# Kernel tuning notes

Hardware: AMD Instinct MI355X
Metric: run time of the kernel (lower is better)

## Reference

```python
import jax, jax.numpy as jnp
import numpy as np

B, T, L, D, H = 8, 8192, 256, 512, 8
HD = D // H  # head_dim = 64


def setup_inputs() -> dict:
    key = jax.random.key(0)
    ks = jax.random.split(key, 6)
    s = 0.02
    return {
        "x": jax.random.normal(ks[0], (B, T, D), jnp.float32),
        "query": jax.random.normal(ks[1], (B, L, D), jnp.float32),
        "Wq": jax.random.normal(ks[2], (D, D), jnp.float32) * s,
        "bq": jnp.zeros((D,), jnp.float32),
        "Wkv": jax.random.normal(ks[3], (D, 2 * D), jnp.float32) * s,
        "bkv": jnp.zeros((2 * D,), jnp.float32),
        "Wproj": jax.random.normal(ks[4], (D, D), jnp.float32) * s,
        "bproj": jnp.zeros((D,), jnp.float32),
    }


def reference(x, query, Wq, bq, Wkv, bkv, Wproj, bproj):
    scale = HD ** (-0.5)
    # projections (weights stored [in, out]; equivalent to torch Linear with W.T)
    q = (query @ Wq + bq).reshape(B, L, H, HD).transpose(0, 2, 1, 3)   # [B,H,L,hd]
    kv = (x @ Wkv + bkv).reshape(B, T, 2, H, HD)
    k = kv[:, :, 0].transpose(0, 2, 1, 3)                              # [B,H,T,hd]
    v = kv[:, :, 1].transpose(0, 2, 1, 3)                              # [B,H,T,hd]
    # scaled dot-product attention, full L x T scores as in original
    attn = jnp.einsum("bhld,bhtd->bhlt", q * scale, k)                 # [B,H,L,T]
    attn = jax.nn.softmax(attn, axis=-1)
    out = jnp.einsum("bhlt,bhtd->bhld", attn, v)                       # [B,H,L,hd]
    out = out.transpose(0, 2, 1, 3).reshape(B, L, D)
    return out @ Wproj + bproj
```

## Files before the change

kernel.cpp:

```cpp
#include <hip/hip_runtime.h>
#include <hip/hip_bf16.h>
#include <cstdint>
#include <cstddef>

typedef __bf16 bf16_t;
typedef __bf16 bf16x8 __attribute__((ext_vector_type(8)));
typedef __bf16 bf16x4 __attribute__((ext_vector_type(4)));
typedef float  f32x4  __attribute__((ext_vector_type(4)));

#define DEVI __device__ __forceinline__

constexpr int B_ = 8, T_ = 8192, L_ = 256, D_ = 512, H_ = 8, HD_ = 64;
constexpr float SCALE_LOG2E = 0.125f * 1.44269504088896340736f;
constexpr int NSPLIT = 4;
constexpr int LOGNS = 2;

DEVI float fast_exp2(float x) {
#if __has_builtin(__builtin_amdgcn_exp2f)
  return __builtin_amdgcn_exp2f(x);
#else
  return exp2f(x);
#endif
}

DEVI void async16(void* lds_base, const void* gptr) {
#if __has_builtin(__builtin_amdgcn_global_load_lds)
  __builtin_amdgcn_global_load_lds(
      (__attribute__((address_space(1))) void*)gptr,
      (__attribute__((address_space(3))) void*)lds_base, 16, 0, 0);
#else
  ((bf16x8*)lds_base)[threadIdx.x & 63] = *(const bf16x8*)gptr;
#endif
}

__global__ __launch_bounds__(256) void prep(
    const float* __restrict__ x,     bf16_t* __restrict__ xb,
    const float* __restrict__ query, bf16_t* __restrict__ qin,
    const float* __restrict__ Wq,    bf16_t* __restrict__ wqT,
    const float* __restrict__ Wkv,   bf16_t* __restrict__ wkvT,
    const float* __restrict__ Wproj, bf16_t* __restrict__ wprojT) {
  __shared__ float tile[32][33];
  const int bid = blockIdx.x;
  const int tid = threadIdx.x;

  if (bid < 4096) {
    const int n4 = (B_ * T_ * D_) / 4;
    const int stride = 4096 * 256;
    for (int i = bid * 256 + tid; i < n4; i += stride) {
      float4 v = ((const float4*)x)[i];
      bf16x4 o;
      o[0] = (bf16_t)v.x; o[1] = (bf16_t)v.y; o[2] = (bf16_t)v.z; o[3] = (bf16_t)v.w;
      ((bf16x4*)xb)[i] = o;
    }
    return;
  }
  if (bid < 4352) {
    const int n4 = (B_ * L_ * D_) / 4;
    const int stride = 256 * 256;
    for (int i = (bid - 4096) * 256 + tid; i < n4; i += stride) {
      float4 v = ((const float4*)query)[i];
      bf16x4 o;
      o[0] = (bf16_t)v.x; o[1] = (bf16_t)v.y; o[2] = (bf16_t)v.z; o[3] = (bf16_t)v.w;
      ((bf16x4*)qin)[i] = o;
    }
    return;
  }

  const float* W; bf16_t* WT; int N; float scale; int idx;
  if (bid < 4608)      { idx = bid - 4352; W = Wq;    WT = wqT;    N = 512;  scale = SCALE_LOG2E; }
  else if (bid < 5120) { idx = bid - 4608; W = Wkv;   WT = wkvT;   N = 1024; scale = 1.0f; }
  else                 { idx = bid - 5120; W = Wproj; WT = wprojT; N = 512;  scale = 1.0f; }
  const int nx = N / 32;
  const int bx = idx % nx, by = idx / nx;
  const int K = 512;
  const int tx = tid & 31, ty = tid >> 5;
  const int n0 = bx * 32, k0 = by * 32;
#pragma unroll
  for (int i = 0; i < 4; ++i)
    tile[ty + i * 8][tx] = W[(size_t)(k0 + ty + i * 8) * N + n0 + tx];
  __syncthreads();
#pragma unroll
  for (int i = 0; i < 4; ++i)
    WT[(size_t)(n0 + ty + i * 8) * K + k0 + tx] = (bf16_t)(tile[tx][ty + i * 8] * scale);
}

template <int MODE>
__global__ __launch_bounds__(256, 4) void gemm_bf16(
    const bf16_t* __restrict__ A, const bf16_t* __restrict__ BT,
    const float* __restrict__ bias, float bscale,
    bf16_t* __restrict__ out0,
    float* __restrict__ outf) {
  constexpr int K = 512;
  __shared__ __align__(16) union SM {
    bf16_t stage[2][128 * 64];
    bf16_t cs[128 * 136];
  } sm;

  const int tid = threadIdx.x;
  const int w = tid >> 6, lane = tid & 63;
  const int m0 = blockIdx.x * 128, n0 = blockIdx.y * 128;
  const int wm = w & 1, wn = w >> 1;

  f32x4 acc[4][4] = {};

  const int sw = ((lane & 7) ^ ((lane >> 3) & 7)) * 8;
  const bf16_t* aG = A + (size_t)(m0 + w * 32 + (lane >> 3)) * K + sw;
  const bf16_t* bG = BT + (size_t)(n0 + w * 32 + (lane >> 3)) * K + sw;
  bf16_t* aL = &sm.stage[0][(w * 32) * 64];
  bf16_t* bL = &sm.stage[1][(w * 32) * 64];

  for (int k0 = 0; k0 < K; k0 += 64) {
#pragma unroll
    for (int i = 0; i < 4; ++i) {
      async16(aL + i * (8 * 64), aG + k0 + (size_t)(i * 8) * K);
      async16(bL + i * (8 * 64), bG + k0 + (size_t)(i * 8) * K);
    }
    __syncthreads();
#pragma unroll
    for (int kk = 0; kk < 2; ++kk) {
      bf16x8 af[4], bfr[4];
      const int cc = ((kk * 4 + (lane >> 4)) ^ (lane & 7)) * 8;
#pragma unroll
      for (int mt = 0; mt < 4; ++mt)
        af[mt] = *(const bf16x8*)&sm.stage[0][(wm * 64 + mt * 16 + (lane & 15)) * 64 + cc];
#pragma unroll
      for (int nt = 0; nt < 4; ++nt)
        bfr[nt] = *(const bf16x8*)&sm.stage[1][(wn * 64 + nt * 16 + (lane & 15)) * 64 + cc];
#pragma unroll
      for (int mt = 0; mt < 4; ++mt)
#pragma unroll
        for (int nt = 0; nt < 4; ++nt)
          acc[mt][nt] = __builtin_amdgcn_mfma_f32_16x16x32_bf16(af[mt], bfr[nt], acc[mt][nt], 0, 0, 0);
    }
    __syncthreads();
  }

  if (MODE == 2) {
#pragma unroll
    for (int nt = 0; nt < 4; ++nt) {
      const int col = n0 + wn * 64 + nt * 16 + (lane & 15);
      const float bv = bias[col];
#pragma unroll
      for (int mt = 0; mt < 4; ++mt)
#pragma unroll
        for (int r = 0; r < 4; ++r) {
          const int row = m0 + wm * 64 + mt * 16 + (lane >> 4) * 4 + r;
          outf[(size_t)row * D_ + col] = acc[mt][nt][r] + bv;
        }
    }
    return;
  }

#pragma unroll
  for (int nt = 0; nt < 4; ++nt) {
    const int col = wn * 64 + nt * 16 + (lane & 15);
    const float bv = bias[n0 + col] * bscale;
#pragma unroll
    for (int mt = 0; mt < 4; ++mt)
#pragma unroll
      for (int r = 0; r < 4; ++r) {
        const int row = wm * 64 + mt * 16 + (lane >> 4) * 4 + r;
        sm.cs[row * 136 + col] = (bf16_t)(acc[mt][nt][r] + bv);
      }
  }
  __syncthreads();

#pragma unroll
  for (int i = 0; i < 8; ++i) {
    const int c = tid + i * 256;
    const int row = c >> 4, col = (c & 15) * 8;
    const int gr = m0 + row;
    const int b = gr >> 8, l = gr & 255;
    const int h = (n0 + col) >> 6, hd = (n0 + col) & 63;
    *(float4*)&out0[((size_t)(b * 8 + h) * L_ + l) * 64 + hd] =
        *(const float4*)&sm.cs[row * 136 + col];
  }
}

__global__ __launch_bounds__(512, 2) void gemm_kv(
    const bf16_t* __restrict__ A, const bf16_t* __restrict__ BT,
    const float* __restrict__ bias,
    bf16_t* __restrict__ kh, bf16_t* __restrict__ vTh) {
  constexpr int K = 512;
  __shared__ __align__(16) union SM {
    bf16_t stage[2][2][256 * 64];
    bf16_t cs[128 * 264];
  } sm;

  const int tid = threadIdx.x;
  const int w = tid >> 6, lane = tid & 63;
  const int wm = w & 1, wn = w >> 1;

  const int b = blockIdx.x;
  const int xcd = b & 7, idx = b >> 3;
  const int m0 = ((xcd << 5) | (idx >> 2)) * 256;
  const int n0 = (idx & 3) * 256;

  f32x4 acc[8][4] = {};

  const int sw = ((lane & 7) ^ ((lane >> 3) & 7)) * 8;
  const bf16_t* aG = A + (size_t)(m0 + w * 8 + (lane >> 3)) * K + sw;
  const bf16_t* bG = BT + (size_t)(n0 + (lane >> 3)) * K + sw;
  bf16_t* SS = &sm.stage[0][0][0];

  const int la = lane & 15;
  const int cc0 = ((lane >> 4) ^ (lane & 7)) * 8;
  const int cc1 = ((4 + (lane >> 4)) ^ (lane & 7)) * 8;

  bf16x8 ra[8], rb[4];

  auto stage_A_half = [&](int bufo, int k0, int h) {
    bf16_t* dA = SS + bufo + (w * 8) * 64;
    const int gb0 = (h == 0) ? 0 : 1;
    const int gb1 = (h == 0) ? 2 : 3;
    async16(dA + (h * 2 + 0) * 4096, aG + k0 + (size_t)(gb0 * 64) * K);
    async16(dA + (h * 2 + 1) * 4096, aG + k0 + (size_t)(gb1 * 64) * K);
  };
  auto stage_B_half = [&](int bufo, int k0, int h) {
    bf16_t* dB = SS + bufo + 16384 + (w * 8) * 64;
#pragma unroll
    for (int j = 0; j < 2; ++j) {
      const int i = h * 2 + j;
      const int r0 = i * 64 + w * 8;
      const int g0 = ((r0 & 127) >> 5) * 64 + (r0 & 31) + (r0 >> 7) * 32;
      async16(dB + i * 4096, bG + k0 + (size_t)g0 * K);
    }
  };
  auto ld_a = [&](const bf16_t* Abase, int mq) {
#pragma unroll
    for (int mt = 0; mt < 4; ++mt) {
      const int rp = mq * 128 + wm * 64 + mt * 16 + la;
      ra[mt * 2]     = *(const bf16x8*)&Abase[rp * 64 + cc0];
      ra[mt * 2 + 1] = *(const bf16x8*)&Abase[rp * 64 + cc1];
    }
  };
  auto ld_b = [&](const bf16_t* Bbase, int nq) {
#pragma unroll
    for (int ntl = 0; ntl < 2; ++ntl) {
      const int rp = nq * 128 + wn * 32 + ntl * 16 + la;
      rb[ntl * 2]     = *(const bf16x8*)&Bbase[rp * 64 + cc0];
      rb[ntl * 2 + 1] = *(const bf16x8*)&Bbase[rp * 64 + cc1];
    }
  };
  auto mm16 = [&](int mq, int nq) {
    __builtin_amdgcn_s_setprio(1);
#pragma unroll
    for (int mt = 0; mt < 4; ++mt)
#pragma unroll
      for (int ntl = 0; ntl < 2; ++ntl) {
        f32x4& c = acc[mq * 4 + mt][nq * 2 + ntl];
        c = __builtin_amdgcn_mfma_f32_16x16x32_bf16(ra[mt * 2],     rb[ntl * 2],     c, 0, 0, 0);
        c = __builtin_amdgcn_mfma_f32_16x16x32_bf16(ra[mt * 2 + 1], rb[ntl * 2 + 1], c, 0, 0, 0);
      }
    __builtin_amdgcn_s_setprio(0);
  };

  stage_A_half(0, 0, 0); stage_B_half(0, 0, 0);
  stage_A_half(0, 0, 1); stage_B_half(0, 0, 1);
  asm volatile("s_waitcnt vmcnt(4)" ::: "memory");
  __builtin_amdgcn_s_barrier();

#pragma unroll
  for (int t = 0; t < 8; ++t) {
    const int Xo = (t & 1) * 32768, Yo = ((t + 1) & 1) * 32768;
    const bf16_t* Ax = SS + Xo;
    const bf16_t* Bx = SS + Xo + 16384;
    ld_a(Ax, 0);
    ld_b(Bx, 0);
    if (t < 7) { stage_A_half(Yo, (t + 1) * 64, 0); stage_B_half(Yo, (t + 1) * 64, 0); }
    __builtin_amdgcn_s_barrier();
    mm16(0, 0);
    if (t < 7) asm volatile("s_waitcnt vmcnt(4)" ::: "memory");
    else       asm volatile("s_waitcnt vmcnt(0)" ::: "memory");
    __builtin_amdgcn_s_barrier();
    ld_b(Bx, 1);
    if (t < 7) { stage_A_half(Yo, (t + 1) * 64, 1); stage_B_half(Yo, (t + 1) * 64, 1); }
    __builtin_amdgcn_s_barrier();
    mm16(0, 1);
    __builtin_amdgcn_s_barrier();
    ld_a(Ax, 1);
    __builtin_amdgcn_s_barrier();
    mm16(1, 1);
    __builtin_amdgcn_s_barrier();
    ld_b(Bx, 0);
    __builtin_amdgcn_s_barrier();
    mm16(1, 0);
    if (t < 7) asm volatile("s_waitcnt vmcnt(4)" ::: "memory");
    __builtin_amdgcn_s_barrier();
  }
  __syncthreads();

  float bv[4];
#pragma unroll
  for (int nt = 0; nt < 4; ++nt)
    bv[nt] = bias[n0 + wn * 64 + nt * 16 + (lane & 15)];

  if (n0 < 512) {
#pragma unroll
    for (int mh = 0; mh < 2; ++mh) {
      if (wm == mh) {
#pragma unroll
        for (int a = 0; a < 8; ++a)
#pragma unroll
          for (int nt = 0; nt < 4; ++nt)
#pragma unroll
            for (int r = 0; r < 4; ++r) {
              const int rowL = a * 16 + (lane >> 4) * 4 + r;
              const int col = wn * 64 + nt * 16 + (lane & 15);
              sm.cs[rowL * 264 + col] = (bf16_t)(acc[a][nt][r] + bv[nt]);
            }
      }
      __syncthreads();
#pragma unroll
      for (int i = 0; i < 8; ++i) {
        const int c = tid + i * 512;
        const int row = c >> 5, col = (c & 31) * 8;
        const int gr = m0 + mh * 128 + row;
        const int bb = gr >> 13, tt = gr & 8191;
        const int h = (n0 + col) >> 6, hd = (n0 + col) & 63;
        *(float4*)&kh[((size_t)(bb * 8 + h) * T_ + tt) * 64 + hd] =
            *(const float4*)&sm.cs[row * 264 + col];
      }
      __syncthreads();
    }
  } else {
    const int bb = m0 >> 13, t0 = m0 & 8191;
#pragma unroll
    for (int nh = 0; nh < 2; ++nh) {
      if ((wn >> 1) == nh) {
#pragma unroll
        for (int a = 0; a < 8; ++a)
#pragma unroll
          for (int nt = 0; nt < 4; ++nt)
#pragma unroll
            for (int r = 0; r < 4; ++r) {
              const int row = wm * 128 + a * 16 + (lane >> 4) * 4 + r;
              const int colL = (wn & 1) * 64 + nt * 16 + (lane & 15);
              sm.cs[colL * 264 + row] = (bf16_t)(acc[a][nt][r] + bv[nt]);
            }
      }
      __syncthreads();
#pragma unroll
      for (int i = 0; i < 8; ++i) {
        const int c = tid + i * 512;
        const int colL = c >> 5, tb = (c & 31) * 8;
        const int ch = (n0 - 512) + nh * 128 + colL;
        const int h = ch >> 6, hd = ch & 63;
        *(float4*)&vTh[((size_t)(bb * 8 + h) * 64 + hd) * T_ + t0 + tb] =
            *(const float4*)&sm.cs[colL * 264 + tb];
      }
      __syncthreads();
    }
  }
}

__global__ __launch_bounds__(256, 4) void attn_fwd(
    const bf16_t* __restrict__ qg, const bf16_t* __restrict__ kg,
    const bf16_t* __restrict__ vg, float* __restrict__ Opart,
    float* __restrict__ lbuf) {
  __shared__ __align__(16) bf16_t KPs[10240];
  __shared__ __align__(16) bf16_t Vs[4 * 64 * 32];
  bf16_t* Ks = KPs;
  bf16_t* Ps = KPs;
  bf16_t* Qs = KPs;

  const int n = blockIdx.x;
  const int split = n & (NSPLIT - 1), qt = (n >> LOGNS) & 3, bh = n >> (LOGNS + 2);
  const int tid = threadIdx.x;
  const int w = tid >> 6, lane = tid & 63;

  {
    const bf16_t* src = qg + ((size_t)bh * L_ + qt * 64) * 64;
    const int row = w * 16 + (lane >> 2);
#pragma unroll
    for (int hh = 0; hh < 2; ++hh)
      async16(&Qs[hh * 2048 + (w * 16) * 32],
              src + (size_t)row * 64 + hh * 32 + (lane & 3) * 8);
  }
  __syncthreads();

  bf16x8 aq[2];
#pragma unroll
  for (int hh = 0; hh < 2; ++hh)
    aq[hh] = *(const bf16x8*)&Qs[hh * 2048 + (w * 16 + (lane & 15)) * 32 + (lane >> 4) * 8];
  __syncthreads();

  bf16x8 ones;
#pragma unroll
  for (int j = 0; j < 8; ++j) ones[j] = (bf16_t)1.0f;

  f32x4 O[4] = {};
  f32x4 lacc = {0.f, 0.f, 0.f, 0.f};

  const int kt0 = split * (T_ / 128 / NSPLIT);
  for (int kt = kt0; kt < kt0 + T_ / 128 / NSPLIT; ++kt) {
#pragma unroll
    for (int hh = 0; hh < 2; ++hh)
#pragma unroll
      for (int i = 0; i < 2; ++i) {
        const int trow = kt * 128 + w * 32 + i * 16 + (lane >> 2);
        async16(&Ks[hh * 4096 + (w * 32 + i * 16) * 32],
                kg + ((size_t)bh * T_ + trow) * 64 + hh * 32 + (lane & 3) * 8);
      }
#pragma unroll
    for (int kc = 0; kc < 4; ++kc) {
      const int hd = w * 16 + (lane >> 2);
      async16(&Vs[kc * 2048 + (w * 16) * 32],
              vg + ((size_t)bh * 64 + hd) * T_ + kt * 128 + kc * 32 + (lane & 3) * 8);
    }
    __syncthreads();

    f32x4 S[8];
#pragma unroll
    for (int nt = 0; nt < 8; ++nt) {
      bf16x8 b0 = *(const bf16x8*)&Ks[0 * 4096 + (nt * 16 + (lane & 15)) * 32 + (lane >> 4) * 8];
      bf16x8 b1 = *(const bf16x8*)&Ks[1 * 4096 + (nt * 16 + (lane & 15)) * 32 + (lane >> 4) * 8];
      f32x4 s = {0.f, 0.f, 0.f, 0.f};
      s = __builtin_amdgcn_mfma_f32_16x16x32_bf16(aq[0], b0, s, 0, 0, 0);
      s = __builtin_amdgcn_mfma_f32_16x16x32_bf16(aq[1], b1, s, 0, 0, 0);
#pragma unroll
      for (int r = 0; r < 4; ++r) s[r] = fast_exp2(s[r]);
      S[nt] = s;
    }

    __syncthreads();

#pragma unroll
    for (int nt = 0; nt < 8; ++nt)
#pragma unroll
      for (int r = 0; r < 4; ++r) {
        const int rp = w * 16 + (lane >> 4) * 4 + r;
        Ps[(nt >> 1) * 2560 + rp * 40 + (nt & 1) * 16 + (lane & 15)] = (bf16_t)S[nt][r];
      }

    __syncthreads();

#pragma unroll
    for (int kc = 0; kc < 4; ++kc) {
      bf16x8 ap = *(const bf16x8*)&Ps[kc * 2560 + (w * 16 + (lane & 15)) * 40 + (lane >> 4) * 8];
      lacc = __builtin_amdgcn_mfma_f32_16x16x32_bf16(ap, ones, lacc, 0, 0, 0);
#pragma unroll
      for (int n2 = 0; n2 < 4; ++n2) {
        bf16x8 bv = *(const bf16x8*)&Vs[kc * 2048 + (n2 * 16 + (lane & 15)) * 32 + (lane >> 4) * 8];
        O[n2] = __builtin_amdgcn_mfma_f32_16x16x32_bf16(ap, bv, O[n2], 0, 0, 0);
      }
    }
    __syncthreads();
  }

  const int part = ((bh * 4 + qt) * NSPLIT + split);
  float* op = Opart + (size_t)part * 64 * 64;
#pragma unroll
  for (int n2 = 0; n2 < 4; ++n2) {
#pragma unroll
    for (int r = 0; r < 4; ++r) {
      const int row = w * 16 + (lane >> 4) * 4 + r;
      op[(size_t)row * 64 + n2 * 16 + (lane & 15)] = O[n2][r];
    }
  }
  if ((lane & 15) == 0) {
    float* lb = lbuf + (size_t)part * 64;
#pragma unroll
    for (int r = 0; r < 4; ++r)
      lb[w * 16 + (lane >> 4) * 4 + r] = lacc[r];
  }
}

__global__ __launch_bounds__(256) void attn_combine(
    const float* __restrict__ Opart, const float* __restrict__ lbuf,
    bf16_t* __restrict__ og) {
  const int blk = blockIdx.x;
  const int bh = blk >> 2, qt = blk & 3;
  const int tid = threadIdx.x;
  const int row = tid >> 2, c0 = (tid & 3) * 16;
  float L = 0.f;
#pragma unroll
  for (int s = 0; s < NSPLIT; ++s) L += lbuf[((size_t)blk * NSPLIT + s) * 64 + row];
  const float inv = 1.f / L;
  f32x4 acc[4] = {};
  const float* ob = Opart + (size_t)blk * NSPLIT * 4096 + row * 64 + c0;
#pragma unroll
  for (int s = 0; s < NSPLIT; ++s)
#pragma unroll
    for (int j = 0; j < 4; ++j) {
      f32x4 v = *(const f32x4*)&ob[s * 4096 + j * 4];
      acc[j] += v;
    }
  const int b = bh >> 3, h = bh & 7;
  bf16_t* dst = og + ((size_t)(b * L_ + qt * 64 + row)) * D_ + h * 64 + c0;
#pragma unroll
  for (int j = 0; j < 4; ++j) {
    bf16x4 o;
#pragma unroll
    for (int e = 0; e < 4; ++e) o[e] = (bf16_t)(acc[j][e] * inv);
    *(bf16x4*)&dst[j * 4] = o;
  }
}

extern "C" void kernel_launch(void* const* d_in, const int* in_sizes, int n_in,
                              void* d_out, int out_size, void* d_ws, size_t ws_size,
                              hipStream_t stream) {
  const float* x     = (const float*)d_in[0];
  const float* query = (const float*)d_in[1];
  const float* Wq    = (const float*)d_in[2];
  const float* bq    = (const float*)d_in[3];
  const float* Wkv   = (const float*)d_in[4];
  const float* bkv   = (const float*)d_in[5];
  const float* Wproj = (const float*)d_in[6];
  const float* bproj = (const float*)d_in[7];
  float* out = (float*)d_out;

  char* ws = (char*)d_ws;
  bf16_t* xb   = (bf16_t*)(ws + 0);
  float*  Opart = (float*)(ws + 0);
  float*  lbuf  = (float*)(ws + 34603008);
  bf16_t* wkvT = (bf16_t*)(ws + 67108864);
  bf16_t* wqT  = (bf16_t*)(ws + 68157440);
  bf16_t* qin  = (bf16_t*)(ws + 68681728);
  bf16_t* qh   = (bf16_t*)(ws + 70778880);
  bf16_t* kh   = (bf16_t*)(ws + 72876032);
  bf16_t* vTh  = (bf16_t*)(ws + 139984896);
  bf16_t* attnb = (bf16_t*)(ws + 207093760);
  bf16_t* wprojT = (bf16_t*)(ws + 209190912);

  prep<<<5376, 256, 0, stream>>>(x, xb, query, qin, Wq, wqT, Wkv, wkvT, Wproj, wprojT);
  gemm_bf16<0><<<dim3(16, 4), 256, 0, stream>>>(qin, wqT, bq, SCALE_LOG2E, qh, nullptr);
  gemm_kv<<<dim3(1024), 512, 0, stream>>>(xb, wkvT, bkv, kh, vTh);
  attn_fwd<<<dim3(64 * 4 * NSPLIT), 256, 0, stream>>>(qh, kh, vTh, Opart, lbuf);
  attn_combine<<<dim3(256), 256, 0, stream>>>(Opart, lbuf, attnb);
  gemm_bf16<2><<<dim3(16, 4), 256, 0, stream>>>(attnb, wprojT, bproj, 1.0f, nullptr, out);
}
```

Measured before the change: 386.9 us.

## Load K and V fragments directly from global memory, dropping LDS staging

The attention kernel no longer stages K and V tiles in shared memory. Each wave now reads its MFMA B-operand fragments for K and V straight from global memory into registers, and the per-iteration __syncthreads barriers go away, since the P buffer is only written and read by the same wave. This cuts LDS usage, which may allow higher occupancy, and removes barrier stalls. In exchange, all four waves redundantly fetch the same K/V tile through the cache hierarchy with strided, less coalesced 16-byte accesses. Removing the barrier after the Q fragment read also creates a possible race between waves reading the shared Q area and waves writing P into the same memory.

```diff
diff --git a/kernel.cpp b/kernel.cpp
--- a/kernel.cpp
+++ b/kernel.cpp
@@ -358,11 +358,8 @@
     const bf16_t* __restrict__ qg, const bf16_t* __restrict__ kg,
     const bf16_t* __restrict__ vg, float* __restrict__ Opart,
     float* __restrict__ lbuf) {
-  __shared__ __align__(16) bf16_t KPs[10240];
-  __shared__ __align__(16) bf16_t Vs[4 * 64 * 32];
-  bf16_t* Ks = KPs;
-  bf16_t* Ps = KPs;
-  bf16_t* Qs = KPs;
+  __shared__ __align__(16) bf16_t Ps[4 * 64 * 40];
+  bf16_t* Qs = Ps;
 
   const int n = blockIdx.x;
   const int split = n & (NSPLIT - 1), qt = (n >> LOGNS) & 3, bh = n >> (LOGNS + 2);
@@ -383,7 +380,6 @@
 #pragma unroll
   for (int hh = 0; hh < 2; ++hh)
     aq[hh] = *(const bf16x8*)&Qs[hh * 2048 + (w * 16 + (lane & 15)) * 32 + (lane >> 4) * 8];
-  __syncthreads();
 
   bf16x8 ones;
 #pragma unroll
@@ -392,29 +388,17 @@
   f32x4 O[4] = {};
   f32x4 lacc = {0.f, 0.f, 0.f, 0.f};
 
+  const bf16_t* kb = kg + (size_t)bh * T_ * 64;
+  const bf16_t* vb = vg + (size_t)bh * 64 * T_;
+
   const int kt0 = split * (T_ / 128 / NSPLIT);
   for (int kt = kt0; kt < kt0 + T_ / 128 / NSPLIT; ++kt) {
-#pragma unroll
-    for (int hh = 0; hh < 2; ++hh)
-#pragma unroll
-      for (int i = 0; i < 2; ++i) {
-        const int trow = kt * 128 + w * 32 + i * 16 + (lane >> 2);
-        async16(&Ks[hh * 4096 + (w * 32 + i * 16) * 32],
-                kg + ((size_t)bh * T_ + trow) * 64 + hh * 32 + (lane & 3) * 8);
-      }
-#pragma unroll
-    for (int kc = 0; kc < 4; ++kc) {
-      const int hd = w * 16 + (lane >> 2);
-      async16(&Vs[kc * 2048 + (w * 16) * 32],
-              vg + ((size_t)bh * 64 + hd) * T_ + kt * 128 + kc * 32 + (lane & 3) * 8);
-    }
-    __syncthreads();
-
+    const bf16_t* krow = kb + (size_t)(kt * 128) * 64 + (lane & 15) * 64 + (lane >> 4) * 8;
     f32x4 S[8];
 #pragma unroll
     for (int nt = 0; nt < 8; ++nt) {
-      bf16x8 b0 = *(const bf16x8*)&Ks[0 * 4096 + (nt * 16 + (lane & 15)) * 32 + (lane >> 4) * 8];
-      bf16x8 b1 = *(const bf16x8*)&Ks[1 * 4096 + (nt * 16 + (lane & 15)) * 32 + (lane >> 4) * 8];
+      bf16x8 b0 = *(const bf16x8*)(krow + nt * (16 * 64));
+      bf16x8 b1 = *(const bf16x8*)(krow + nt * (16 * 64) + 32);
       f32x4 s = {0.f, 0.f, 0.f, 0.f};
       s = __builtin_amdgcn_mfma_f32_16x16x32_bf16(aq[0], b0, s, 0, 0, 0);
       s = __builtin_amdgcn_mfma_f32_16x16x32_bf16(aq[1], b1, s, 0, 0, 0);
@@ -423,8 +407,6 @@
       S[nt] = s;
     }
 
-    __syncthreads();
-
 #pragma unroll
     for (int nt = 0; nt < 8; ++nt)
 #pragma unroll
@@ -433,19 +415,17 @@
         Ps[(nt >> 1) * 2560 + rp * 40 + (nt & 1) * 16 + (lane & 15)] = (bf16_t)S[nt][r];
       }
 
-    __syncthreads();
-
+    const bf16_t* vrow = vb + (size_t)(lane & 15) * T_ + kt * 128 + (lane >> 4) * 8;
 #pragma unroll
     for (int kc = 0; kc < 4; ++kc) {
       bf16x8 ap = *(const bf16x8*)&Ps[kc * 2560 + (w * 16 + (lane & 15)) * 40 + (lane >> 4) * 8];
       lacc = __builtin_amdgcn_mfma_f32_16x16x32_bf16(ap, ones, lacc, 0, 0, 0);
 #pragma unroll
       for (int n2 = 0; n2 < 4; ++n2) {
-        bf16x8 bv = *(const bf16x8*)&Vs[kc * 2048 + (n2 * 16 + (lane & 15)) * 32 + (lane >> 4) * 8];
+        bf16x8 bv = *(const bf16x8*)(vrow + (size_t)(n2 * 16) * T_ + kc * 32);
         O[n2] = __builtin_amdgcn_mfma_f32_16x16x32_bf16(ap, bv, O[n2], 0, 0, 0);
       }
     }
-    __syncthreads();
   }
 
   const int part = ((bh * 4 + qt) * NSPLIT + split);
```

Result: slower. 538.3 us (+39.2%).
